# Kernel optimization log

Measured on AMD Instinct MI355X. Metric: run time of the kernel, lower is better.

## Reference

```python
import jax, jax.numpy as jnp
import numpy as np
import math

L = 2      # num_patient_encoder_layers
NE = 4     # number of note-type experts
H = 768    # hidden_size
FF = 4 * H # dim_feedforward
NH = H // 64  # num heads
HD = 64       # head dim
B, S = 8, 256
EPS = 1e-5


def setup_inputs() -> dict:
    key = jax.random.key(0)
    ks = jax.random.split(key, 12)
    std = 0.02
    x = jax.random.normal(ks[0], (B, S, H), dtype=jnp.float32)
    # all notes valid; note_pos values are 1..B*S so order_notes is an identity permutation
    note_pos = (jnp.arange(B * S, dtype=jnp.int64) + 1).reshape(B, S)
    note_type_pos = jax.random.randint(ks[1], (B * S,), 0, NE)
    Wq = jax.random.normal(ks[2], (L, H, H), dtype=jnp.float32) * std
    Wk = jax.random.normal(ks[3], (L, H, H), dtype=jnp.float32) * std
    Wv = jax.random.normal(ks[4], (L, H, H), dtype=jnp.float32) * std
    bq = jnp.zeros((L, H), jnp.float32)
    bk = jnp.zeros((L, H), jnp.float32)
    bv = jnp.zeros((L, H), jnp.float32)
    ln1_w = jnp.ones((L, H), jnp.float32)
    ln1_b = jnp.zeros((L, H), jnp.float32)
    ln2_w = jnp.ones((L, H), jnp.float32)
    ln2_b = jnp.zeros((L, H), jnp.float32)
    W1 = jax.random.normal(ks[5], (L, NE, H, FF), dtype=jnp.float32) * std
    b1 = jnp.zeros((L, NE, FF), jnp.float32)
    W2 = jax.random.normal(ks[6], (L, NE, FF, H), dtype=jnp.float32) * std
    b2 = jnp.zeros((L, NE, H), jnp.float32)
    return dict(x=x, note_pos=note_pos, note_type_pos=note_type_pos,
                Wq=Wq, bq=bq, Wk=Wk, bk=bk, Wv=Wv, bv=bv,
                ln1_w=ln1_w, ln1_b=ln1_b, ln2_w=ln2_w, ln2_b=ln2_b,
                W1=W1, b1=b1, W2=W2, b2=b2)


def _layer_norm(x, w, b):
    mu = jnp.mean(x, axis=-1, keepdims=True)
    var = jnp.mean(jnp.square(x - mu), axis=-1, keepdims=True)
    return (x - mu) * jax.lax.rsqrt(var + EPS) * w + b


def _sinusoidal_pe(seq_len, d_model):
    pos = jnp.arange(seq_len, dtype=jnp.float32)[:, None]
    div = jnp.exp(jnp.arange(0, d_model, 2, dtype=jnp.float32) * (-math.log(10000.0) / d_model))
    ang = pos * div  # [S, H/2]
    # interleave sin at even, cos at odd indices
    return jnp.stack([jnp.sin(ang), jnp.cos(ang)], axis=-1).reshape(seq_len, d_model)


def reference(x, note_pos, note_type_pos, Wq, bq, Wk, bk, Wv, bv,
              ln1_w, ln1_b, ln2_w, ln2_b, W1, b1, W2, b2):
    Bc, Sc, Hc = x.shape
    x = x + _sinusoidal_pe(Sc, Hc)[None]
    attn_mask = (note_pos != 0).astype(x.dtype)                 # [B, S]
    add_mask = (1.0 - attn_mask)[:, None, None, :] * -10000.0    # [B,1,1,S]
    flat_idx = note_pos.reshape(-1)                              # identity perm, values 1..B*S

    for l in range(L):
        # --- self attention (no 1/sqrt(d) scaling, as in source) ---
        h = _layer_norm(x, ln1_w[l], ln1_b[l])
        q = (h @ Wq[l] + bq[l]).reshape(Bc, Sc, NH, HD)
        k = (h @ Wk[l] + bk[l]).reshape(Bc, Sc, NH, HD)
        v = (h @ Wv[l] + bv[l]).reshape(Bc, Sc, NH, HD)
        scores = jnp.einsum('bqhd,bkhd->bhqk', q, k) + add_mask
        probs = jax.nn.softmax(scores, axis=-1)
        ctx = jnp.einsum('bhqk,bkhd->bqhd', probs, v).reshape(Bc, Sc, Hc)
        x = x + ctx

        # --- gather valid notes to flat token list (identity here) ---
        xf = x.reshape(-1, Hc)                                   # [T, H]
        hf = _layer_norm(xf, ln2_w[l], ln2_b[l])
        # --- note-type routed expert FFN ---
        out = jnp.zeros_like(xf)
        for e in range(NE):
            he = jax.nn.gelu(hf @ W1[l, e] + b1[l, e], approximate=False) @ W2[l, e] + b2[l, e]
            out = jnp.where((note_type_pos == e)[:, None], he, out)
        xf = xf + out
        # --- scatter back via order_notes: pad zero row, gather by note_pos ---
        padded = jnp.concatenate([jnp.zeros((1, Hc), xf.dtype), xf], axis=0)
        x = padded[flat_idx].reshape(Bc, Sc, Hc)
    return x
```

## Files before the change

### kernel.cpp

```cpp
#include <hip/hip_runtime.h>

typedef __bf16 bf16_t;
typedef __attribute__((ext_vector_type(8))) __bf16 bf16x8;
typedef __attribute__((ext_vector_type(4))) float f32x4;

static constexpr int Lc = 2, NEc = 4, Hc = 768, FFc = 3072, NHc = 12;
static constexpr int Bc = 8, Tc = 2048;

__device__ __forceinline__ void gll16(const bf16_t* g, bf16_t* l) {
  __builtin_amdgcn_global_load_lds(
      (const __attribute__((address_space(1))) void*)g,
      (__attribute__((address_space(3))) void*)l, 16, 0, 0);
}

__global__ __launch_bounds__(64) void route_k(const int* __restrict__ ntp,
                                              int* __restrict__ perm,
                                              int* __restrict__ offs) {
  int lane = threadIdx.x;
  int myE[32];
  int cnt0 = 0, cnt1 = 0, cnt2 = 0, cnt3 = 0;
  for (int c = 0; c < 32; ++c) {
    int e = ntp[c * 64 + lane];
    myE[c] = e;
    cnt0 += __popcll(__ballot(e == 0));
    cnt1 += __popcll(__ballot(e == 1));
    cnt2 += __popcll(__ballot(e == 2));
    cnt3 += __popcll(__ballot(e == 3));
  }
  int b0 = 0, b1 = cnt0, b2 = cnt0 + cnt1, b3 = cnt0 + cnt1 + cnt2;
  if (lane == 0) {
    offs[0] = 0; offs[1] = b1; offs[2] = b2; offs[3] = b3; offs[4] = b3 + cnt3;
  }
  unsigned long long below = (lane == 63) ? ~0ull >> 1 : ((1ull << lane) - 1);
  for (int c = 0; c < 32; ++c) {
    int e = myE[c];
    unsigned long long m0 = __ballot(e == 0), m1 = __ballot(e == 1);
    unsigned long long m2 = __ballot(e == 2), m3 = __ballot(e == 3);
    unsigned long long mm = (e == 0) ? m0 : (e == 1) ? m1 : (e == 2) ? m2 : m3;
    int base = (e == 0) ? b0 : (e == 1) ? b1 : (e == 2) ? b2 : b3;
    perm[base + __popcll(mm & below)] = c * 64 + lane;
    b0 += __popcll(m0); b1 += __popcll(m1); b2 += __popcll(m2); b3 += __popcll(m3);
  }
}

__global__ __launch_bounds__(256) void pe_add(const float* __restrict__ xin,
                                              float* __restrict__ x0) {
  int p = blockIdx.x * 256 + threadIdx.x;
  int t = p / 384;
  int jj = p - t * 384;
  int s = t & 255;
  float ang = (float)s * __expf((float)jj * -0.0239852613894f);
  float sn, cs;
  sincosf(ang, &sn, &cs);
  float2 xv = ((const float2*)xin)[p];
  float2 o;  o.x = xv.x + sn;  o.y = xv.y + cs;
  ((float2*)x0)[p] = o;
}

__global__ __launch_bounds__(256) void ln_k(const float* __restrict__ x,
                                            const float* __restrict__ g,
                                            const float* __restrict__ bb,
                                            bf16_t* __restrict__ out) {
  int w = threadIdx.x >> 6, lane = threadIdx.x & 63;
  int t = blockIdx.x * 4 + w;
  const float4* xr = (const float4*)(x + (size_t)t * Hc);
  float4 v[3];
  float s = 0.f, s2 = 0.f;
  for (int i = 0; i < 3; ++i) {
    v[i] = xr[lane + i * 64];
    s  += v[i].x + v[i].y + v[i].z + v[i].w;
    s2 += v[i].x * v[i].x + v[i].y * v[i].y + v[i].z * v[i].z + v[i].w * v[i].w;
  }
  for (int o = 1; o < 64; o <<= 1) { s += __shfl_xor(s, o); s2 += __shfl_xor(s2, o); }
  float mu = s * (1.f / 768.f);
  float r = rsqrtf(s2 * (1.f / 768.f) - mu * mu + 1e-5f);
  bf16_t* orow = out + (size_t)t * Hc;
  for (int i = 0; i < 3; ++i) {
    int i4 = lane + i * 64;
    float4 gg = ((const float4*)g)[i4];
    float4 b4 = ((const float4*)bb)[i4];
    union { bf16_t h[4]; uint2 u; } pk;
    pk.h[0] = (bf16_t)((v[i].x - mu) * r * gg.x + b4.x);
    pk.h[1] = (bf16_t)((v[i].y - mu) * r * gg.y + b4.y);
    pk.h[2] = (bf16_t)((v[i].z - mu) * r * gg.z + b4.z);
    pk.h[3] = (bf16_t)((v[i].w - mu) * r * gg.w + b4.w);
    ((uint2*)orow)[i4] = pk.u;
  }
}

__global__ __launch_bounds__(256) void tconv(const float* __restrict__ s0,
                                             const float* __restrict__ s1,
                                             const float* __restrict__ s2,
                                             int mdiv, long sls, long sms,
                                             bf16_t* __restrict__ dst, long dls, long dms,
                                             int K, int N) {
  int z = blockIdx.z;
  int l = z / mdiv, m = z % mdiv;
  const float* src;
  if (s1) src = (m == 0 ? s0 : (m == 1 ? s1 : s2)) + (size_t)l * sls;
  else src = s0 + (size_t)l * sls + (size_t)m * sms;
  bf16_t* d = dst + (size_t)l * dls + (size_t)m * dms;
  int n0 = blockIdx.x * 64, k0 = blockIdx.y * 64;
  __shared__ float tl[64][65];
  int c = threadIdx.x & 63, r0 = threadIdx.x >> 6;
  for (int i = 0; i < 16; ++i) {
    int r = r0 + i * 4;
    tl[r][c] = src[(size_t)(k0 + r) * N + n0 + c];
  }
  __syncthreads();
  for (int i = 0; i < 16; ++i) {
    int r = r0 + i * 4;
    d[(size_t)(n0 + r) * K + k0 + c] = (bf16_t)tl[c][r];
  }
}

template <int MODE, int BN>
__global__ __launch_bounds__(256) void gemm2(
    const bf16_t* __restrict__ A, const bf16_t* __restrict__ Bt,
    int K, int N, int kIters, long btStride, long biasStride,
    const int* __restrict__ perm, const int* __restrict__ offs,
    const float* __restrict__ bqp, const float* __restrict__ bkp,
    const float* __restrict__ bvp, const float* __restrict__ biasE,
    float* __restrict__ outF, bf16_t* __restrict__ outB) {
  constexpr int TN = BN / 32;
  constexpr int BCH = BN / 64;
  __shared__ bf16_t Ald[128 * 32];
  __shared__ bf16_t Bld[BN * 32];
  int tid = threadIdx.x, lane = tid & 63, w = tid >> 6;
  int quad = lane >> 4, col = lane & 15;
  int m0 = blockIdx.y * 128, n0 = blockIdx.x * BN;
  int e = 0, ks = 0, kStart = 0, off = 0, cnt = Tc;
  if (MODE == 1) e = blockIdx.z;
  if (MODE == 2) { e = blockIdx.z >> 1; ks = blockIdx.z & 1; kStart = ks * (K / 2); }
  if (MODE != 0) {
    off = offs[e];
    cnt = offs[e + 1] - off;
    if (m0 >= cnt) return;
  }
  const bf16_t* B0 = Bt + (size_t)e * btStride;

  const bf16_t* ga[2];
  bf16_t* la[2];
  for (int j = 0; j < 2; ++j) {
    int rbase = 32 * w + 16 * j;
    int row = rbase + (lane >> 2);
    int ch = ((lane & 3) - (row >> 1)) & 3;
    int gm = m0 + row;
    int gmc = (gm < cnt) ? gm : (cnt - 1);
    int srow;
    if (MODE == 0) srow = gm;
    else if (MODE == 1) srow = perm[off + gmc];
    else srow = off + gmc;
    ga[j] = A + (size_t)srow * K + kStart + ch * 8;
    la[j] = Ald + rbase * 32;
  }
  const bf16_t* gb[BCH];
  bf16_t* lb[BCH];
  for (int j = 0; j < BCH; ++j) {
    int rbase = (BCH == 2) ? (32 * w + 16 * j) : (16 * w);
    int row = rbase + (lane >> 2);
    int ch = ((lane & 3) - (row >> 1)) & 3;
    gb[j] = B0 + (size_t)(n0 + row) * K + kStart + ch * 8;
    lb[j] = Bld + rbase * 32;
  }

  int wr = (w >> 1) * 64, wc = (w & 1) * (BN / 2);
  const bf16_t* ar[4];
  const bf16_t* br[TN];
  for (int r = 0; r < 4; ++r) {
    int row = wr + r * 16 + col;
    ar[r] = Ald + row * 32 + (((quad + (row >> 1)) & 3) << 3);
  }
  for (int c = 0; c < TN; ++c) {
    int row = wc + c * 16 + col;
    br[c] = Bld + row * 32 + (((quad + (row >> 1)) & 3) << 3);
  }

  const f32x4 z4 = {0.f, 0.f, 0.f, 0.f};
  f32x4 acc[4][TN];
  for (int r = 0; r < 4; ++r)
    for (int c = 0; c < TN; ++c) acc[r][c] = z4;

  for (int it = 0; it < kIters; ++it) {
    __syncthreads();
    gll16(ga[0], la[0]);
    gll16(ga[1], la[1]);
    for (int j = 0; j < BCH; ++j) gll16(gb[j], lb[j]);
    ga[0] += 32; ga[1] += 32;
    for (int j = 0; j < BCH; ++j) gb[j] += 32;
    __syncthreads();
    bf16x8 af[4], bv[TN];
    for (int r = 0; r < 4; ++r) af[r] = *(const bf16x8*)ar[r];
    for (int c = 0; c < TN; ++c) bv[c] = *(const bf16x8*)br[c];
    for (int r = 0; r < 4; ++r)
      for (int c = 0; c < TN; ++c)
        acc[r][c] = __builtin_amdgcn_mfma_f32_16x16x32_bf16(af[r], bv[c], acc[r][c], 0, 0, 0);
  }

  for (int r = 0; r < 4; ++r)
    for (int c = 0; c < TN; ++c) {
      int mloc = wr + r * 16 + quad * 4;
      int n = n0 + wc + c * 16 + col;
      for (int i = 0; i < 4; ++i) {
        int gm = m0 + mloc + i;
        float av = acc[r][c][i];
        if (MODE == 0) {
          float bias = (n < 768) ? bqp[n] : (n < 1536) ? bkp[n - 768] : bvp[n - 1536];
          outB[(size_t)gm * N + n] = (bf16_t)(av + bias);
        } else if (MODE == 1) {
          if (gm < cnt) {
            float v = av + biasE[(size_t)e * biasStride + n];
            float u = v * (0.7978845608f + 0.0356774081f * v * v);
            float t = 1.f - 2.f / (1.f + __expf(2.f * u));
            outB[(size_t)(off + gm) * N + n] = (bf16_t)(0.5f * v * (1.f + t));
          }
        } else {
          if (gm < cnt) {
            int tok = perm[off + gm];
            outF[(size_t)ks * Tc * Hc + (size_t)tok * N + n] = av;
          }
        }
      }
    }
}

__global__ __launch_bounds__(256) void attn_k(const bf16_t* __restrict__ qkv,
                                              const int* __restrict__ np,
                                              float* __restrict__ x) {
  __shared__ bf16_t Kld[256 * 64];
  __shared__ bf16_t Vt[64 * 256];
  int tid = threadIdx.x, lane = tid & 63, w = tid >> 6;
  int qt = blockIdx.x;
  int b = blockIdx.y / NHc, h = blockIdx.y % NHc;

  for (int j = 0; j < 8; ++j) {
    int rbase = w * 64 + j * 8;
    int row = rbase + (lane >> 3);
    int oc = ((lane & 7) - row) & 7;
    const bf16_t* gp = qkv + ((size_t)(b * 256 + row)) * 2304 + 768 + h * 64 + oc * 8;
    gll16(gp, Kld + rbase * 64);
  }
  {
    int s = tid, shi = s >> 3, slo = s & 7;
    const uint4* vs = (const uint4*)(qkv + ((size_t)(b * 256 + s)) * 2304 + 1536 + h * 64);
    for (int cc = 0; cc < 8; ++cc) {
      uint4 pk = vs[cc];
      const bf16_t* pv = (const bf16_t*)&pk;
      for (int jj = 0; jj < 8; ++jj) {
        int d = cc * 8 + jj;
        Vt[d * 256 + ((shi + d) & 31) * 8 + slo] = pv[jj];
      }
    }
  }
  int quad = lane >> 4, col = lane & 15;
  float madd[16];
  for (int nt = 0; nt < 16; ++nt)
    madd[nt] = (np[b * 256 + nt * 16 + col] != 0) ? 0.f : -10000.f;
  int qrow = qt * 64 + w * 16 + col;
  const bf16_t* qb = qkv + ((size_t)(b * 256 + qrow)) * 2304 + h * 64;
  bf16x8 qf0 = *(const bf16x8*)(qb + quad * 8);
  bf16x8 qf1 = *(const bf16x8*)(qb + 32 + quad * 8);
  __syncthreads();

  const f32x4 z4 = {0.f, 0.f, 0.f, 0.f};
  f32x4 sc[16];
  for (int nt = 0; nt < 16; ++nt) {
    int row = nt * 16 + col;
    bf16x8 k0 = *(const bf16x8*)(Kld + row * 64 + (((0 + quad + row) & 7) << 3));
    bf16x8 k1 = *(const bf16x8*)(Kld + row * 64 + (((4 + quad + row) & 7) << 3));
    f32x4 z = z4;
    z = __builtin_amdgcn_mfma_f32_16x16x32_bf16(qf0, k0, z, 0, 0, 0);
    z = __builtin_amdgcn_mfma_f32_16x16x32_bf16(qf1, k1, z, 0, 0, 0);
    sc[nt] = z;
  }
  for (int nt = 0; nt < 16; ++nt) {
    float a = madd[nt];
    sc[nt][0] += a; sc[nt][1] += a; sc[nt][2] += a; sc[nt][3] += a;
  }
  float pm[4], rl[4];
  for (int i = 0; i < 4; ++i) {
    float m = -1e30f;
    for (int nt = 0; nt < 16; ++nt) m = fmaxf(m, sc[nt][i]);
    for (int o = 1; o < 16; o <<= 1) m = fmaxf(m, __shfl_xor(m, o));
    float ssum = 0.f;
    for (int nt = 0; nt < 16; ++nt) ssum += __expf(sc[nt][i] - m);
    for (int o = 1; o < 16; o <<= 1) ssum += __shfl_xor(ssum, o);
    pm[i] = m;
    rl[i] = 1.f / ssum;
  }
  __syncthreads();
  bf16_t* Pb = Kld + w * 4096;
  for (int nt = 0; nt < 16; ++nt)
    for (int i = 0; i < 4; ++i) {
      int prow = quad * 4 + i;
      int key = nt * 16 + col;
      Pb[prow * 256 + (((key >> 3) + prow) & 31) * 8 + (key & 7)] =
          (bf16_t)__expf(sc[nt][i] - pm[i]);
    }
  __syncthreads();
  f32x4 oacc[4];
  for (int i = 0; i < 4; ++i) oacc[i] = z4;
  for (int kk2 = 0; kk2 < 8; ++kk2) {
    bf16x8 pa = *(const bf16x8*)(Pb + col * 256 + (((kk2 * 4 + quad + col) & 31) << 3));
    for (int nt2 = 0; nt2 < 4; ++nt2) {
      int d = nt2 * 16 + col;
      bf16x8 bv8 = *(const bf16x8*)(Vt + d * 256 + (((kk2 * 4 + quad + d) & 31) << 3));
      oacc[nt2] = __builtin_amdgcn_mfma_f32_16x16x32_bf16(pa, bv8, oacc[nt2], 0, 0, 0);
    }
  }
  for (int nt2 = 0; nt2 < 4; ++nt2)
    for (int i = 0; i < 4; ++i) {
      size_t o = ((size_t)(b * 256 + qt * 64 + w * 16 + quad * 4 + i)) * Hc + h * 64 + nt2 * 16 + col;
      x[o] += oacc[nt2][i] * rl[i];
    }
}

__global__ __launch_bounds__(256) void combine_k(const float* __restrict__ x0,
                                                 const float* __restrict__ pbuf,
                                                 const float* __restrict__ b2l,
                                                 const int* __restrict__ ntp,
                                                 const int* __restrict__ np,
                                                 float* __restrict__ dst) {
  int i = blockIdx.x * 256 + threadIdx.x;
  int t = i / 192, d = i - t * 192;
  int idx = np[t];
  float4 o;
  if (idx != 0) {
    int r = idx - 1;
    int e = ntp[r];
    size_t j = (size_t)r * 192 + d;
    float4 a = ((const float4*)x0)[j];
    float4 p0 = ((const float4*)pbuf)[j];
    float4 p1 = ((const float4*)pbuf)[(size_t)Tc * 192 + j];
    float4 bb = ((const float4*)(b2l + (size_t)e * Hc))[d];
    o.x = a.x + p0.x + p1.x + bb.x;
    o.y = a.y + p0.y + p1.y + bb.y;
    o.z = a.z + p0.z + p1.z + bb.z;
    o.w = a.w + p0.w + p1.w + bb.w;
  } else {
    o.x = o.y = o.z = o.w = 0.f;
  }
  ((float4*)dst)[i] = o;
}

extern "C" void kernel_launch(void* const* d_in, const int* in_sizes, int n_in,
                              void* d_out, int out_size, void* d_ws, size_t ws_size,
                              hipStream_t stream) {
  const float* x_in = (const float*)d_in[0];
  const int* note_pos = (const int*)d_in[1];
  const int* ntp = (const int*)d_in[2];
  const float* Wq = (const float*)d_in[3];
  const float* bq = (const float*)d_in[4];
  const float* Wk = (const float*)d_in[5];
  const float* bk = (const float*)d_in[6];
  const float* Wv = (const float*)d_in[7];
  const float* bv = (const float*)d_in[8];
  const float* ln1w = (const float*)d_in[9];
  const float* ln1b = (const float*)d_in[10];
  const float* ln2w = (const float*)d_in[11];
  const float* ln2b = (const float*)d_in[12];
  const float* W1 = (const float*)d_in[13];
  const float* b1 = (const float*)d_in[14];
  const float* W2 = (const float*)d_in[15];
  const float* b2 = (const float*)d_in[16];
  float* out = (float*)d_out;

  char* p = (char*)d_ws;
  auto carve = [&](size_t bytes) -> char* {
    char* r = p;
    p += (bytes + 255) & ~(size_t)255;
    return r;
  };
  float* xA = (float*)carve((size_t)Tc * Hc * 4);
  float* xB = (float*)carve((size_t)Tc * Hc * 4);
  float* pbuf = (float*)carve((size_t)2 * Tc * Hc * 4);
  bf16_t* h16 = (bf16_t*)carve((size_t)Tc * Hc * 2);
  bf16_t* big = (bf16_t*)carve((size_t)Tc * FFc * 2);
  bf16_t* qkv16 = big;
  bf16_t* act1 = big;
  bf16_t* wqkvt = (bf16_t*)carve((size_t)Lc * 2304 * 768 * 2);
  bf16_t* w1t = (bf16_t*)carve((size_t)Lc * NEc * FFc * Hc * 2);
  bf16_t* w2t = (bf16_t*)carve((size_t)Lc * NEc * Hc * FFc * 2);
  int* perm = (int*)carve(Tc * 4);
  int* offs = (int*)carve(64);

  route_k<<<1, 64, 0, stream>>>(ntp, perm, offs);
  pe_add<<<Tc * Hc / 2 / 256, 256, 0, stream>>>(x_in, xA);

  tconv<<<dim3(12, 12, 6), 256, 0, stream>>>(Wq, Wk, Wv, 3, (long)Hc * Hc, 0L,
                                             wqkvt, (long)2304 * 768, (long)Hc * Hc, Hc, Hc);
  tconv<<<dim3(48, 12, 8), 256, 0, stream>>>(W1, nullptr, nullptr, 4,
                                             (long)NEc * Hc * FFc, (long)Hc * FFc,
                                             w1t, (long)NEc * FFc * Hc, (long)FFc * Hc, Hc, FFc);
  tconv<<<dim3(12, 48, 8), 256, 0, stream>>>(W2, nullptr, nullptr, 4,
                                             (long)NEc * FFc * Hc, (long)FFc * Hc,
                                             w2t, (long)NEc * Hc * FFc, (long)Hc * FFc, FFc, Hc);

  float* xcur = xA;
  for (int l = 0; l < Lc; ++l) {
    float* xdst = (l == Lc - 1) ? out : xB;
    ln_k<<<Tc / 4, 256, 0, stream>>>(xcur, ln1w + l * Hc, ln1b + l * Hc, h16);
    gemm2<0, 64><<<dim3(36, 16, 1), 256, 0, stream>>>(
        h16, wqkvt + (size_t)l * 2304 * 768, Hc, 2304, 24, 0L, 0L, perm, offs,
        bq + l * Hc, bk + l * Hc, bv + l * Hc, nullptr, nullptr, qkv16);
    attn_k<<<dim3(4, Bc * NHc), 256, 0, stream>>>(qkv16, note_pos, xcur);
    ln_k<<<Tc / 4, 256, 0, stream>>>(xcur, ln2w + l * Hc, ln2b + l * Hc, h16);
    gemm2<1, 64><<<dim3(48, 16, NEc), 256, 0, stream>>>(
        h16, w1t + (size_t)l * NEc * FFc * Hc, Hc, FFc, 24, (long)FFc * Hc, (long)FFc,
        perm, offs, nullptr, nullptr, nullptr, b1 + (size_t)l * NEc * FFc, nullptr, act1);
    gemm2<2, 64><<<dim3(12, 16, NEc * 2), 256, 0, stream>>>(
        act1, w2t + (size_t)l * NEc * Hc * FFc, FFc, Hc, 48, (long)Hc * FFc, 0L,
        perm, offs, nullptr, nullptr, nullptr, nullptr, pbuf, nullptr);
    combine_k<<<Tc * 192 / 256, 256, 0, stream>>>(xcur, pbuf, b2 + (size_t)l * NEc * Hc,
                                                  ntp, note_pos, xdst);
    float* tmp = xcur; xcur = xdst; xB = tmp;
  }
}
```

Baseline: 486.5 us.

## Deepen GEMM K-tile to 64 and make M-tile a template parameter

The GEMM kernel now stages a 64-wide K slice per iteration instead of 32, using an 8-chunk XOR swizzle in LDS and two MFMA sub-steps per barrier pair. This halves the number of sync/load rounds. The M tile becomes a template parameter, so the second FFN GEMM runs with 64-row tiles across twice as many blocks, which helps it keep more CUs busy on small expert groups. LDS use per block goes up, which may lower occupancy.

```diff
diff --git a/kernel.cpp b/kernel.cpp
--- a/kernel.cpp
+++ b/kernel.cpp
@@ -114,7 +114,7 @@
   }
 }
 
-template <int MODE, int BN>
+template <int MODE, int BM>
 __global__ __launch_bounds__(256) void gemm2(
     const bf16_t* __restrict__ A, const bf16_t* __restrict__ Bt,
     int K, int N, int kIters, long btStride, long biasStride,
@@ -122,13 +122,14 @@
     const float* __restrict__ bqp, const float* __restrict__ bkp,
     const float* __restrict__ bvp, const float* __restrict__ biasE,
     float* __restrict__ outF, bf16_t* __restrict__ outB) {
-  constexpr int TN = BN / 32;
-  constexpr int BCH = BN / 64;
-  __shared__ bf16_t Ald[128 * 32];
-  __shared__ bf16_t Bld[BN * 32];
+  constexpr int TM = BM / 32;
+  constexpr int TN = 2;
+  constexpr int AI = BM / 32;
+  __shared__ bf16_t Ald[BM * 64];
+  __shared__ bf16_t Bld[64 * 64];
   int tid = threadIdx.x, lane = tid & 63, w = tid >> 6;
   int quad = lane >> 4, col = lane & 15;
-  int m0 = blockIdx.y * 128, n0 = blockIdx.x * BN;
+  int m0 = blockIdx.y * BM, n0 = blockIdx.x * 64;
   int e = 0, ks = 0, kStart = 0, off = 0, cnt = Tc;
   if (MODE == 1) e = blockIdx.z;
   if (MODE == 2) { e = blockIdx.z >> 1; ks = blockIdx.z & 1; kStart = ks * (K / 2); }
@@ -139,12 +140,12 @@
   }
   const bf16_t* B0 = Bt + (size_t)e * btStride;
 
-  const bf16_t* ga[2];
-  bf16_t* la[2];
-  for (int j = 0; j < 2; ++j) {
-    int rbase = 32 * w + 16 * j;
-    int row = rbase + (lane >> 2);
-    int ch = ((lane & 3) - (row >> 1)) & 3;
+  const bf16_t* ga[AI];
+  bf16_t* la[AI];
+  for (int j = 0; j < AI; ++j) {
+    int rbase = w * (BM / 4) + j * 8;
+    int row = rbase + (lane >> 3);
+    int ch = ((lane & 7) - row) & 7;
     int gm = m0 + row;
     int gmc = (gm < cnt) ? gm : (cnt - 1);
     int srow;
@@ -152,52 +153,52 @@
     else if (MODE == 1) srow = perm[off + gmc];
     else srow = off + gmc;
     ga[j] = A + (size_t)srow * K + kStart + ch * 8;
-    la[j] = Ald + rbase * 32;
-  }
-  const bf16_t* gb[BCH];
-  bf16_t* lb[BCH];
-  for (int j = 0; j < BCH; ++j) {
-    int rbase = (BCH == 2) ? (32 * w + 16 * j) : (16 * w);
-    int row = rbase + (lane >> 2);
-    int ch = ((lane & 3) - (row >> 1)) & 3;
+    la[j] = Ald + rbase * 64;
+  }
+  const bf16_t* gb[2];
+  bf16_t* lb[2];
+  for (int j = 0; j < 2; ++j) {
+    int rbase = w * 16 + j * 8;
+    int row = rbase + (lane >> 3);
+    int ch = ((lane & 7) - row) & 7;
     gb[j] = B0 + (size_t)(n0 + row) * K + kStart + ch * 8;
-    lb[j] = Bld + rbase * 32;
-  }
-
-  int wr = (w >> 1) * 64, wc = (w & 1) * (BN / 2);
-  const bf16_t* ar[4];
-  const bf16_t* br[TN];
-  for (int r = 0; r < 4; ++r) {
+    lb[j] = Bld + rbase * 64;
+  }
+
+  int wr = (w >> 1) * (BM / 2), wc = (w & 1) * 32;
+  int aoff[TM], boff[TN];
+  for (int r = 0; r < TM; ++r) {
     int row = wr + r * 16 + col;
-    ar[r] = Ald + row * 32 + (((quad + (row >> 1)) & 3) << 3);
+    aoff[r] = row * 64 + (((quad + row) & 7) << 3);
   }
   for (int c = 0; c < TN; ++c) {
     int row = wc + c * 16 + col;
-    br[c] = Bld + row * 32 + (((quad + (row >> 1)) & 3) << 3);
+    boff[c] = row * 64 + (((quad + row) & 7) << 3);
   }
 
   const f32x4 z4 = {0.f, 0.f, 0.f, 0.f};
-  f32x4 acc[4][TN];
-  for (int r = 0; r < 4; ++r)
+  f32x4 acc[TM][TN];
+  for (int r = 0; r < TM; ++r)
     for (int c = 0; c < TN; ++c) acc[r][c] = z4;
 
   for (int it = 0; it < kIters; ++it) {
     __syncthreads();
-    gll16(ga[0], la[0]);
-    gll16(ga[1], la[1]);
-    for (int j = 0; j < BCH; ++j) gll16(gb[j], lb[j]);
-    ga[0] += 32; ga[1] += 32;
-    for (int j = 0; j < BCH; ++j) gb[j] += 32;
+    for (int j = 0; j < AI; ++j) gll16(ga[j], la[j]);
+    for (int j = 0; j < 2; ++j) gll16(gb[j], lb[j]);
+    for (int j = 0; j < AI; ++j) ga[j] += 64;
+    for (int j = 0; j < 2; ++j) gb[j] += 64;
     __syncthreads();
-    bf16x8 af[4], bv[TN];
-    for (int r = 0; r < 4; ++r) af[r] = *(const bf16x8*)ar[r];
-    for (int c = 0; c < TN; ++c) bv[c] = *(const bf16x8*)br[c];
-    for (int r = 0; r < 4; ++r)
-      for (int c = 0; c < TN; ++c)
-        acc[r][c] = __builtin_amdgcn_mfma_f32_16x16x32_bf16(af[r], bv[c], acc[r][c], 0, 0, 0);
-  }
-
-  for (int r = 0; r < 4; ++r)
+    for (int kk = 0; kk < 2; ++kk) {
+      bf16x8 af[TM], bv[TN];
+      for (int r = 0; r < TM; ++r) af[r] = *(const bf16x8*)(Ald + (aoff[r] ^ (kk << 5)));
+      for (int c = 0; c < TN; ++c) bv[c] = *(const bf16x8*)(Bld + (boff[c] ^ (kk << 5)));
+      for (int r = 0; r < TM; ++r)
+        for (int c = 0; c < TN; ++c)
+          acc[r][c] = __builtin_amdgcn_mfma_f32_16x16x32_bf16(af[r], bv[c], acc[r][c], 0, 0, 0);
+    }
+  }
+
+  for (int r = 0; r < TM; ++r)
     for (int c = 0; c < TN; ++c) {
       int mloc = wr + r * 16 + quad * 4;
       int n = n0 + wc + c * 16 + col;
@@ -400,16 +401,16 @@
   for (int l = 0; l < Lc; ++l) {
     float* xdst = (l == Lc - 1) ? out : xB;
     ln_k<<<Tc / 4, 256, 0, stream>>>(xcur, ln1w + l * Hc, ln1b + l * Hc, h16);
-    gemm2<0, 64><<<dim3(36, 16, 1), 256, 0, stream>>>(
-        h16, wqkvt + (size_t)l * 2304 * 768, Hc, 2304, 24, 0L, 0L, perm, offs,
+    gemm2<0, 128><<<dim3(36, 16, 1), 256, 0, stream>>>(
+        h16, wqkvt + (size_t)l * 2304 * 768, Hc, 2304, 12, 0L, 0L, perm, offs,
         bq + l * Hc, bk + l * Hc, bv + l * Hc, nullptr, nullptr, qkv16);
     attn_k<<<dim3(4, Bc * NHc), 256, 0, stream>>>(qkv16, note_pos, xcur);
     ln_k<<<Tc / 4, 256, 0, stream>>>(xcur, ln2w + l * Hc, ln2b + l * Hc, h16);
-    gemm2<1, 64><<<dim3(48, 16, NEc), 256, 0, stream>>>(
-        h16, w1t + (size_t)l * NEc * FFc * Hc, Hc, FFc, 24, (long)FFc * Hc, (long)FFc,
+    gemm2<1, 128><<<dim3(48, 16, NEc), 256, 0, stream>>>(
+        h16, w1t + (size_t)l * NEc * FFc * Hc, Hc, FFc, 12, (long)FFc * Hc, (long)FFc,
         perm, offs, nullptr, nullptr, nullptr, b1 + (size_t)l * NEc * FFc, nullptr, act1);
-    gemm2<2, 64><<<dim3(12, 16, NEc * 2), 256, 0, stream>>>(
-        act1, w2t + (size_t)l * NEc * Hc * FFc, FFc, Hc, 48, (long)Hc * FFc, 0L,
+    gemm2<2, 64><<<dim3(12, 32, NEc * 2), 256, 0, stream>>>(
+        act1, w2t + (size_t)l * NEc * Hc * FFc, FFc, Hc, 24, (long)Hc * FFc, 0L,
         perm, offs, nullptr, nullptr, nullptr, nullptr, pbuf, nullptr);
     combine_k<<<Tc * 192 / 256, 256, 0, stream>>>(xcur, pbuf, b2 + (size_t)l * NEc * Hc,
                                                   ntp, note_pos, xdst);
```

Result: faster. 454.6 us (-6.5%).
